# Optimization experiments

Hardware: AMD Instinct MI355X
Metric: run time of the kernel (lower is better)

Reference implementation:

```python
import jax, jax.numpy as jnp
import numpy as np

STRIDE = 1

def setup_inputs() -> dict:
    key = jax.random.key(0)
    k1, k2 = jax.random.split(key)
    x = jax.random.normal(k1, (64, 16384), dtype=jnp.float32)        # (B, L)
    kernel = jax.random.normal(k2, (128, 16), dtype=jnp.float32) * 0.05  # (F, K) == phi
    return {"x": x, "kernel": kernel}

def reference(x, kernel):
    # Faithful math of SpecCnn1d_v01.call: the sparse phi places kernel[f, j]
    # at (f, i, i*stride + j), so phi @ x^T == windowed dot product.
    B, L = x.shape
    F, K = kernel.shape
    out_len = (L - K) // STRIDE + 1  # floor((L + 2*0 - K)/stride) + 1
    # Sliding windows: (out_len, K) gather indices -> windows (B, out_len, K)
    idx = jnp.arange(out_len)[:, None] * STRIDE + jnp.arange(K)[None, :]
    windows = x[:, idx]                       # (B, O, K)
    y = jnp.einsum('bok,fk->bof', windows, kernel)  # (B, O, F), matches perm [2,1,0]
    return jax.nn.relu(y)                     # activation='relu', use_bias=False
```

## Files before the change

kernel.cpp:

```cpp
#include <hip/hip_runtime.h>


constexpr int K_TAPS  = 16;
constexpr int F_FILT  = 128;
constexpr int O_TILE  = 64;
constexpr int O_CHUNK = 8;

__global__ __launch_bounds__(F_FILT) void SpecCnn1d_conv_kernel(
    const float* __restrict__ x,
    const float* __restrict__ w,
    float* __restrict__ y,
    int L, int out_len)
{
    const int f  = threadIdx.x;
    const int b  = blockIdx.y;
    const int o0 = blockIdx.x * O_TILE;

    float wr[K_TAPS];
    const float4* w4 = reinterpret_cast<const float4*>(w + f * K_TAPS);
    #pragma unroll
    for (int i = 0; i < K_TAPS / 4; ++i) {
        float4 v = w4[i];
        wr[4 * i + 0] = v.x;
        wr[4 * i + 1] = v.y;
        wr[4 * i + 2] = v.z;
        wr[4 * i + 3] = v.w;
    }

    const float* xb = x + (size_t)b * L;
    float*       yb = y + ((size_t)b * out_len + o0) * F_FILT + f;

    for (int oc = 0; oc < O_TILE; oc += O_CHUNK) {
        const int base = o0 + oc;

        float xs[O_CHUNK + K_TAPS - 1];
        #pragma unroll
        for (int j = 0; j < O_CHUNK + K_TAPS - 1; ++j) {
            int xi = base + j;
            xi = (xi < L) ? xi : (L - 1);
            xs[j] = xb[xi];
        }

        #pragma unroll
        for (int oo = 0; oo < O_CHUNK; ++oo) {
            float acc = 0.0f;
            #pragma unroll
            for (int k = 0; k < K_TAPS; ++k)
                acc = fmaf(xs[oo + k], wr[k], acc);
            const int o = base + oo;
            if (o < out_len)
                yb[(size_t)(oc + oo) * F_FILT] = fmaxf(acc, 0.0f);
        }
    }
}

extern "C" void kernel_launch(void* const* d_in, const int* in_sizes, int n_in,
                              void* d_out, int out_size, void* d_ws, size_t ws_size,
                              hipStream_t stream) {
    const float* x = (const float*)d_in[0];
    const float* w = (const float*)d_in[1];
    float*       y = (float*)d_out;

    const int B = 64;
    const int L = in_sizes[0] / B;
    const int out_len = L - K_TAPS + 1;

    dim3 grid((out_len + O_TILE - 1) / O_TILE, B);
    dim3 block(F_FILT);
    SpecCnn1d_conv_kernel<<<grid, block, 0, stream>>>(x, w, y, L, out_len);
}
```

Before: 543.9 us.

## Compute four filters per thread with vectorized float4 loads and stores

Restructures the thread mapping so each thread computes 4 adjacent filters for 8 outputs, with 256-thread blocks split into 8 output groups. Input windows are loaded with float4 and outputs are written as float4, cutting the instruction count per byte stored. It raises register use (64 weights) and sets launch bounds to keep occupancy.

```diff
diff --git a/kernel.cpp b/kernel.cpp
--- a/kernel.cpp
+++ b/kernel.cpp
@@ -1,55 +1,71 @@
 #include <hip/hip_runtime.h>
 
 
-constexpr int K_TAPS  = 16;
-constexpr int F_FILT  = 128;
-constexpr int O_TILE  = 64;
-constexpr int O_CHUNK = 8;
+constexpr int K_TAPS = 16;
+constexpr int F_FILT = 128;
+constexpr int O_PER_THREAD = 8;
+constexpr int O_TILE = 64;
 
-__global__ __launch_bounds__(F_FILT) void SpecCnn1d_conv_kernel(
+__global__ __launch_bounds__(256, 4) void SpecCnn1d_conv_kernel(
     const float* __restrict__ x,
     const float* __restrict__ w,
     float* __restrict__ y,
     int L, int out_len)
 {
-    const int f  = threadIdx.x;
-    const int b  = blockIdx.y;
-    const int o0 = blockIdx.x * O_TILE;
+    const int tid    = threadIdx.x;
+    const int fg     = (tid & 31) * 4;
+    const int og     = tid >> 5;
+    const int b      = blockIdx.y;
+    const int o_base = blockIdx.x * O_TILE + og * O_PER_THREAD;
 
-    float wr[K_TAPS];
-    const float4* w4 = reinterpret_cast<const float4*>(w + f * K_TAPS);
+    float wr[4][K_TAPS];
     #pragma unroll
-    for (int i = 0; i < K_TAPS / 4; ++i) {
-        float4 v = w4[i];
-        wr[4 * i + 0] = v.x;
-        wr[4 * i + 1] = v.y;
-        wr[4 * i + 2] = v.z;
-        wr[4 * i + 3] = v.w;
+    for (int ff = 0; ff < 4; ++ff) {
+        const float4* w4 = reinterpret_cast<const float4*>(w + (fg + ff) * K_TAPS);
+        #pragma unroll
+        for (int i = 0; i < K_TAPS / 4; ++i) {
+            float4 v = w4[i];
+            wr[ff][4*i+0] = v.x; wr[ff][4*i+1] = v.y;
+            wr[ff][4*i+2] = v.z; wr[ff][4*i+3] = v.w;
+        }
     }
 
     const float* xb = x + (size_t)b * L;
-    float*       yb = y + ((size_t)b * out_len + o0) * F_FILT + f;
+    float xs[O_PER_THREAD + K_TAPS];
+    if (o_base + 23 < L) {
+        const float4* x4 = reinterpret_cast<const float4*>(xb + o_base);
+        #pragma unroll
+        for (int i = 0; i < 6; ++i) {
+            float4 v = x4[i];
+            xs[4*i+0] = v.x; xs[4*i+1] = v.y; xs[4*i+2] = v.z; xs[4*i+3] = v.w;
+        }
+    } else {
+        #pragma unroll
+        for (int j = 0; j < 24; ++j) {
+            int xi = o_base + j;
+            xs[j] = xb[(xi < L) ? xi : (L - 1)];
+        }
+    }
 
-    for (int oc = 0; oc < O_TILE; oc += O_CHUNK) {
-        const int base = o0 + oc;
+    float* yb = y + (size_t)b * out_len * F_FILT + fg;
 
-        float xs[O_CHUNK + K_TAPS - 1];
+    #pragma unroll
+    for (int i = 0; i < O_PER_THREAD; ++i) {
+        float a0 = 0.f, a1 = 0.f, a2 = 0.f, a3 = 0.f;
         #pragma unroll
-        for (int j = 0; j < O_CHUNK + K_TAPS - 1; ++j) {
-            int xi = base + j;
-            xi = (xi < L) ? xi : (L - 1);
-            xs[j] = xb[xi];
+        for (int k = 0; k < K_TAPS; ++k) {
+            const float xv = xs[i + k];
+            a0 = fmaf(xv, wr[0][k], a0);
+            a1 = fmaf(xv, wr[1][k], a1);
+            a2 = fmaf(xv, wr[2][k], a2);
+            a3 = fmaf(xv, wr[3][k], a3);
         }
-
-        #pragma unroll
-        for (int oo = 0; oo < O_CHUNK; ++oo) {
-            float acc = 0.0f;
-            #pragma unroll
-            for (int k = 0; k < K_TAPS; ++k)
-                acc = fmaf(xs[oo + k], wr[k], acc);
-            const int o = base + oo;
-            if (o < out_len)
-                yb[(size_t)(oc + oo) * F_FILT] = fmaxf(acc, 0.0f);
+        const int o = o_base + i;
+        if (o < out_len) {
+            float4 r;
+            r.x = fmaxf(a0, 0.f); r.y = fmaxf(a1, 0.f);
+            r.z = fmaxf(a2, 0.f); r.w = fmaxf(a3, 0.f);
+            *reinterpret_cast<float4*>(yb + (size_t)o * F_FILT) = r;
         }
     }
 }
@@ -66,6 +82,6 @@
     const int out_len = L - K_TAPS + 1;
 
     dim3 grid((out_len + O_TILE - 1) / O_TILE, B);
-    dim3 block(F_FILT);
+    dim3 block(256);
     SpecCnn1d_conv_kernel<<<grid, block, 0, stream>>>(x, w, y, L, out_len);
 }
```

Result: slower. 585.8 us (+7.7%).
